# Kernel optimization log

Hardware: AMD Instinct MI355X
Metric: run time of the kernel (lower is better)

Reference implementation:

```python
import jax, jax.numpy as jnp
import numpy as np

D_MODEL = 1024
N_HEADS = 16
MAX_LAG = 512
D_K = D_MODEL // N_HEADS


def setup_inputs() -> dict:
    key = jax.random.key(0)
    ks = jax.random.split(key, 11)
    B, S = 2, 2048
    x = jax.random.normal(ks[0], (B, S, D_MODEL), dtype=jnp.float32)
    lag = jax.random.randint(ks[1], (S,), 0, MAX_LAG + 1, dtype=jnp.int64)
    scale = 1.0 / np.sqrt(D_MODEL)
    wq = jax.random.normal(ks[2], (D_MODEL, D_MODEL), dtype=jnp.float32) * scale
    bq = jnp.zeros((D_MODEL,), dtype=jnp.float32)
    wk = jax.random.normal(ks[3], (D_MODEL, D_MODEL), dtype=jnp.float32) * scale
    bk = jnp.zeros((D_MODEL,), dtype=jnp.float32)
    wv = jax.random.normal(ks[4], (D_MODEL, D_MODEL), dtype=jnp.float32) * scale
    bv = jnp.zeros((D_MODEL,), dtype=jnp.float32)
    wo = jax.random.normal(ks[5], (D_MODEL, D_MODEL), dtype=jnp.float32) * scale
    bo = jnp.zeros((D_MODEL,), dtype=jnp.float32)
    lag_bias = jax.random.normal(ks[6], (N_HEADS, MAX_LAG + 1), dtype=jnp.float32) * 0.02
    return {"x": x, "lag": lag, "wq": wq, "bq": bq, "wk": wk, "bk": bk,
            "wv": wv, "bv": bv, "wo": wo, "bo": bo, "lag_bias": lag_bias}


def reference(x, lag, wq, bq, wk, bk, wv, bv, wo, bo, lag_bias):
    B, S, D = x.shape
    H, dk = N_HEADS, D_K
    # projections: torch Linear is x @ W.T + b; here weights stored as (in, out)
    q = (x @ wq + bq).reshape(B, S, H, dk).transpose(0, 2, 1, 3)  # (B,H,S,dk)
    k = (x @ wk + bk).reshape(B, S, H, dk).transpose(0, 2, 1, 3)
    v = (x @ wv + bv).reshape(B, S, H, dk).transpose(0, 2, 1, 3)
    scores = jnp.einsum('bhqd,bhkd->bhqk', q, k) / jnp.sqrt(jnp.float32(dk))
    ld = jnp.abs(lag[:, None] - lag[None, :]).astype(jnp.int32)  # (S,S)
    bias = lag_bias[:, ld]  # (H,S,S)
    attn = jax.nn.softmax(scores + bias[None], axis=-1)
    out = jnp.einsum('bhqk,bhkd->bhqd', attn, v)
    out = out.transpose(0, 2, 1, 3).reshape(B, S, D)
    return out @ wo + bo
```

## Files before the change

kernel.cpp:

```cpp
#include <hip/hip_runtime.h>

typedef __bf16 bf16;
typedef __bf16 bf16x8 __attribute__((ext_vector_type(8)));
typedef float f32x4 __attribute__((ext_vector_type(4)));

__device__ __forceinline__ f32x4 mfma16(bf16x8 a, bf16x8 b, f32x4 c) {
  return __builtin_amdgcn_mfma_f32_16x16x32_bf16(a, b, c, 0, 0, 0);
}
__device__ __forceinline__ void gload16(const bf16* g, bf16* l) {
  __builtin_amdgcn_global_load_lds((const __attribute__((address_space(1))) unsigned int*)g,
                                   (__attribute__((address_space(3))) unsigned int*)l, 16, 0, 0);
}

__global__ __launch_bounds__(256) void cvt_x_kernel(const float* __restrict__ in,
                                                    bf16* __restrict__ out, int n8) {
  int i = blockIdx.x * 256 + threadIdx.x;
  if (i >= n8) return;
  const float4* p = (const float4*)in + (size_t)i * 2;
  float4 f0 = p[0], f1 = p[1];
  bf16x8 o;
  o[0] = (bf16)f0.x; o[1] = (bf16)f0.y; o[2] = (bf16)f0.z; o[3] = (bf16)f0.w;
  o[4] = (bf16)f1.x; o[5] = (bf16)f1.y; o[6] = (bf16)f1.z; o[7] = (bf16)f1.w;
  *((bf16x8*)out + i) = o;
}

__global__ __launch_bounds__(256) void cvt_wt_kernel(const float* __restrict__ in,
                                                     bf16* __restrict__ out) {
  __shared__ float t[64][68];
  int bx = blockIdx.x & 15;
  int by = blockIdx.x >> 4;
  int tid = threadIdx.x;
  int r = tid >> 2, p = tid & 3;
  const float* src = in + (size_t)(by * 64 + r) * 1024 + bx * 64 + p * 16;
#pragma unroll
  for (int j = 0; j < 16; j += 4)
    *(float4*)&t[r][p * 16 + j] = *(const float4*)(src + j);
  __syncthreads();
  int n = tid >> 2, sp = tid & 3;
  bf16 tmp[16];
#pragma unroll
  for (int j = 0; j < 16; ++j) tmp[j] = (bf16)t[sp * 16 + j][n];
  bf16* dst = out + (size_t)(bx * 64 + n) * 1024 + by * 64 + sp * 16;
  *(bf16x8*)dst = *(bf16x8*)&tmp[0];
  *(bf16x8*)(dst + 8) = *(bf16x8*)&tmp[8];
}

__global__ void cvt_bias_kernel(const float* __restrict__ bq, const float* __restrict__ bk,
                                const float* __restrict__ bv, float* __restrict__ out) {
  int i = blockIdx.x * 256 + threadIdx.x;
  if (i < 1024) out[i] = bq[i];
  else if (i < 2048) out[i] = bk[i - 1024];
  else if (i < 3072) out[i] = bv[i - 2048];
}

__global__ __launch_bounds__(256) void sort_lag_kernel(const int* __restrict__ lag,
                                                       int* __restrict__ perm,
                                                       int* __restrict__ slag) {
  __shared__ int l[2048];
  int tid = threadIdx.x;
  for (int i = tid; i < 2048; i += 256) l[i] = lag[i];
  __syncthreads();
  int i = blockIdx.x * 32 + (tid >> 3);
  int s = tid & 7;
  int vi = l[i];
  int cnt = 0;
  for (int j = s * 256; j < s * 256 + 256; j += 4) {
    int4 vj = *(const int4*)&l[j];
    cnt += (vj.x < vi || (vj.x == vi && (j + 0) < i));
    cnt += (vj.y < vi || (vj.y == vi && (j + 1) < i));
    cnt += (vj.z < vi || (vj.z == vi && (j + 2) < i));
    cnt += (vj.w < vi || (vj.w == vi && (j + 3) < i));
  }
  cnt += __shfl_xor(cnt, 1);
  cnt += __shfl_xor(cnt, 2);
  cnt += __shfl_xor(cnt, 4);
  if (s == 0) { perm[cnt] = i; slag[cnt] = vi; }
}

__global__ __launch_bounds__(256) void pack_kv_kernel(const bf16* __restrict__ qkv,
                                                      const int* __restrict__ perm,
                                                      bf16* __restrict__ kp,
                                                      bf16* __restrict__ vt) {
  __shared__ bf16 t[64][72];
  int blk = blockIdx.x;
  int st = blk & 31, h = (blk >> 5) & 15, b = blk >> 9;
  int tid = threadIdx.x;
  int r = tid >> 2, p = tid & 3;
  int src_s = perm[st * 64 + r];
  {
    const bf16* src = qkv + (size_t)(b * 2048 + src_s) * 3072 + 1024 + h * 64 + p * 16;
    bf16* dst = kp + (size_t)((b * 16 + h) * 2048 + st * 64 + r) * 64 + p * 16;
    *(bf16x8*)dst = *(const bf16x8*)src;
    *(bf16x8*)(dst + 8) = *(const bf16x8*)(src + 8);
  }
  {
    const bf16* src = qkv + (size_t)(b * 2048 + src_s) * 3072 + 2048 + h * 64 + p * 16;
    *(bf16x8*)&t[r][p * 16] = *(const bf16x8*)src;
    *(bf16x8*)&t[r][p * 16 + 8] = *(const bf16x8*)(src + 8);
    __syncthreads();
    int d = tid >> 2, sp = tid & 3;
    bf16 tmp[16];
#pragma unroll
    for (int j = 0; j < 16; ++j) tmp[j] = t[sp * 16 + j][d];
    bf16* dst = vt + (size_t)((b * 16 + h) * 64 + d) * 2048 + st * 64 + sp * 16;
    *(bf16x8*)dst = *(bf16x8*)&tmp[0];
    *(bf16x8*)(dst + 8) = *(bf16x8*)&tmp[8];
  }
}

template <int OUT_BF16>
__global__ __launch_bounds__(256) void gemm_bt_kernel(
    const bf16* __restrict__ A, const bf16* __restrict__ Bt,
    const float* __restrict__ bias, void* __restrict__ C,
    int M, int N, int K, int scale_cols, float scale_val) {
  __shared__ __align__(16) bf16 As[128 * 64];
  __shared__ __align__(16) bf16 Bs[128 * 64];
  int bn = blockIdx.x * 128, bm = blockIdx.y * 128;
  int tid = threadIdx.x;
  int l = tid & 63;
  int w = tid >> 6;
  int wr = w >> 1, wc = w & 1;
  int g = l >> 4, c = l & 15;
  int swz = (c & 7) << 3;
  int srow = l >> 3;
  int scol = ((l & 7) ^ srow) << 3;
  const bf16* Ap = A + (size_t)(bm + w * 32 + srow) * K + scol;
  const bf16* Bp = Bt + (size_t)(bn + w * 32 + srow) * K + scol;
  bf16* AsW = As + w * 32 * 64;
  bf16* BsW = Bs + w * 32 * 64;

  f32x4 acc[4][4] = {};
  for (int k0 = 0; k0 < K; k0 += 64) {
    __syncthreads();
#pragma unroll
    for (int i = 0; i < 4; ++i) {
      gload16(Ap + (size_t)(8 * i) * K + k0, AsW + i * 512);
      gload16(Bp + (size_t)(8 * i) * K + k0, BsW + i * 512);
    }
    __syncthreads();
#pragma unroll
    for (int kh = 0; kh < 2; ++kh) {
      bf16x8 af[4], bfr[4];
#pragma unroll
      for (int m = 0; m < 4; ++m)
        af[m] = *(const bf16x8*)&As[(wr * 64 + m * 16 + c) * 64 + ((kh * 32 + g * 8) ^ swz)];
#pragma unroll
      for (int n = 0; n < 4; ++n)
        bfr[n] = *(const bf16x8*)&Bs[(wc * 64 + n * 16 + c) * 64 + ((kh * 32 + g * 8) ^ swz)];
#pragma unroll
      for (int m = 0; m < 4; ++m)
#pragma unroll
        for (int n = 0; n < 4; ++n)
          acc[m][n] = mfma16(af[m], bfr[n], acc[m][n]);
    }
  }
  int rowb = bm + wr * 64;
  int colb = bn + wc * 64;
#pragma unroll
  for (int n = 0; n < 4; ++n) {
    int col = colb + n * 16 + c;
    float bv = bias[col];
    float s = (col < scale_cols) ? scale_val : 1.0f;
#pragma unroll
    for (int m = 0; m < 4; ++m) {
      int row = rowb + m * 16 + g * 4;
#pragma unroll
      for (int j = 0; j < 4; ++j) {
        float v = (acc[m][n][j] + bv) * s;
        if (OUT_BF16)
          ((bf16*)C)[(size_t)(row + j) * N + col] = (bf16)v;
        else
          ((float*)C)[(size_t)(row + j) * N + col] = v;
      }
    }
  }
}

__global__ __launch_bounds__(256) void attn_kernel(
    const bf16* __restrict__ qkv, const bf16* __restrict__ kp,
    const bf16* __restrict__ vt, const int* __restrict__ lag,
    const int* __restrict__ slag, const float* __restrict__ lag_bias,
    bf16* __restrict__ out) {
  __shared__ __align__(16) bf16 Ks0[64 * 64];
  __shared__ __align__(16) bf16 Vs0[64 * 64];
  __shared__ __align__(16) bf16 Ks1[64 * 64];
  __shared__ __align__(16) bf16 Vs1[64 * 64];
  __shared__ __align__(16) bf16 Ps[4][32][72];
  __shared__ float bias_s[516];
  __shared__ int lag_s[2048];

  int blk = blockIdx.x;
  blk = (blk & 7) * 64 + (blk >> 3);
  int qt = blk & 15;
  int h = (blk >> 4) & 15;
  int b = blk >> 8;
  int tid = threadIdx.x;
  int w = tid >> 6, l = tid & 63, g = l >> 4, c = l & 15;

  for (int i = tid; i < 513; i += 256) bias_s[i] = lag_bias[h * 513 + i] * 1.44269504f;
  for (int i = tid; i < 2048; i += 256) lag_s[i] = slag[i];

  int q0 = qt * 128 + w * 32;
  const bf16* qbase = qkv + (size_t)(b * 2048 + q0) * 3072 + h * 64;
  bf16x8 qf[2][2];
#pragma unroll
  for (int m = 0; m < 2; ++m)
#pragma unroll
    for (int kh = 0; kh < 2; ++kh)
      qf[m][kh] = *(const bf16x8*)(qbase + (size_t)(m * 16 + c) * 3072 + kh * 32 + g * 8);

  int lagq[2][4];
#pragma unroll
  for (int m = 0; m < 2; ++m)
#pragma unroll
    for (int j = 0; j < 4; ++j) lagq[m][j] = lag[q0 + m * 16 + g * 4 + j];

  int swz = (c & 7) << 3;
  int off0 = (g * 8) ^ swz;
  int off1 = off0 ^ 32;

  int r0 = w * 16 + (l >> 3);
  int colE = ((l & 7) ^ (l >> 3)) << 3;
  const bf16* kbase = kp + (size_t)(b * 16 + h) * 2048 * 64;
  const bf16* vbase = vt + (size_t)(b * 16 + h) * 64 * 2048;
  const bf16* kg0 = kbase + (size_t)r0 * 64 + colE;
  const bf16* kg1 = kbase + (size_t)(r0 + 8) * 64 + colE;
  const bf16* vg0 = vbase + (size_t)r0 * 2048 + colE;
  const bf16* vg1 = vbase + (size_t)(r0 + 8) * 2048 + colE;

#define STAGE(KD, VD)                    \
  do {                                   \
    gload16(kg0, KD + w * 1024);         \
    gload16(kg1, KD + w * 1024 + 512);   \
    gload16(vg0, VD + w * 1024);         \
    gload16(vg1, VD + w * 1024 + 512);   \
    kg0 += 64 * 64; kg1 += 64 * 64;      \
    vg0 += 64; vg1 += 64;                \
  } while (0)

  STAGE(Ks0, Vs0);
  __syncthreads();

  f32x4 oacc[2][4] = {};
  float psum[2][4] = {};

#define TILE(KB, VB, KT)                                                          \
  do {                                                                            \
    f32x4 sf[2][4] = {};                                                          \
    int lagk[4];                                                                  \
    _Pragma("unroll") for (int kb = 0; kb < 4; ++kb) {                            \
      int row = kb * 16 + c;                                                      \
      bf16x8 k0 = *(const bf16x8*)&KB[row * 64 + off0];                           \
      bf16x8 k1 = *(const bf16x8*)&KB[row * 64 + off1];                           \
      sf[0][kb] = mfma16(qf[0][0], k0, sf[0][kb]);                                \
      sf[0][kb] = mfma16(qf[0][1], k1, sf[0][kb]);                                \
      sf[1][kb] = mfma16(qf[1][0], k0, sf[1][kb]);                                \
      sf[1][kb] = mfma16(qf[1][1], k1, sf[1][kb]);                                \
      lagk[kb] = lag_s[(KT) + kb * 16 + c];                                       \
    }                                                                             \
    _Pragma("unroll") for (int m = 0; m < 2; ++m)                                 \
    _Pragma("unroll") for (int kb = 0; kb < 4; ++kb)                              \
    _Pragma("unroll") for (int j = 0; j < 4; ++j) {                               \
      int ld = lagq[m][j] - lagk[kb];                                             \
      ld = ld < 0 ? -ld : ld;                                                     \
      float p = __builtin_amdgcn_exp2f(sf[m][kb][j] + bias_s[ld]);                \
      psum[m][j] += p;                                                            \
      Ps[w][m * 16 + g * 4 + j][kb * 16 + c] = (bf16)p;                           \
    }                                                                             \
    asm volatile("s_waitcnt lgkmcnt(0)" ::: "memory");                            \
    _Pragma("unroll") for (int ph = 0; ph < 2; ++ph) {                            \
      bf16x8 pa0 = *(const bf16x8*)&Ps[w][c][ph * 32 + g * 8];                    \
      bf16x8 pa1 = *(const bf16x8*)&Ps[w][16 + c][ph * 32 + g * 8];               \
      int voff = ph ? off1 : off0;                                                \
      _Pragma("unroll") for (int n = 0; n < 4; ++n) {                             \
        bf16x8 vf = *(const bf16x8*)&VB[(n * 16 + c) * 64 + voff];                \
        oacc[0][n] = mfma16(pa0, vf, oacc[0][n]);                                 \
        oacc[1][n] = mfma16(pa1, vf, oacc[1][n]);                                 \
      }                                                                           \
    }                                                                             \
  } while (0)

  for (int kt = 0; kt < 2048; kt += 128) {
    if (kt + 64 < 2048) STAGE(Ks1, Vs1);
    TILE(Ks0, Vs0, kt);
    __syncthreads();
    if (kt + 128 < 2048) STAGE(Ks0, Vs0);
    TILE(Ks1, Vs1, kt + 64);
    __syncthreads();
  }

#pragma unroll
  for (int m = 0; m < 2; ++m) {
#pragma unroll
    for (int j = 0; j < 4; ++j) {
      float s = psum[m][j];
      s += __shfl_xor(s, 1);
      s += __shfl_xor(s, 2);
      s += __shfl_xor(s, 4);
      s += __shfl_xor(s, 8);
      float inv = 1.f / s;
      bf16* ob = out + (size_t)(b * 2048 + q0 + m * 16 + g * 4 + j) * 1024 + h * 64;
#pragma unroll
      for (int n = 0; n < 4; ++n)
        ob[n * 16 + c] = (bf16)(oacc[m][n][j] * inv);
    }
  }
#undef STAGE
#undef TILE
}

extern "C" void kernel_launch(void* const* d_in, const int* in_sizes, int n_in,
                              void* d_out, int out_size, void* d_ws, size_t ws_size,
                              hipStream_t stream) {
  const float* x        = (const float*)d_in[0];
  const int*   lag      = (const int*)d_in[1];
  const float* wq       = (const float*)d_in[2];
  const float* bq       = (const float*)d_in[3];
  const float* wk       = (const float*)d_in[4];
  const float* bk       = (const float*)d_in[5];
  const float* wv       = (const float*)d_in[6];
  const float* bv       = (const float*)d_in[7];
  const float* wo       = (const float*)d_in[8];
  const float* bo       = (const float*)d_in[9];
  const float* lag_bias = (const float*)d_in[10];

  char* ws = (char*)d_ws;
  bf16*  xb    = (bf16*)ws;
  bf16*  wqkvt = (bf16*)(ws + (8u  << 20));
  bf16*  wot   = (bf16*)(ws + (14u << 20));
  float* bqkv  = (float*)(ws + (16u << 20));
  int*   perm  = (int*)(ws + (16u << 20) + 32768);
  int*   slag  = (int*)(ws + (16u << 20) + 65536);
  bf16*  qkv   = (bf16*)(ws + (17u << 20));
  bf16*  vtb   = (bf16*)(ws + (41u << 20));
  bf16*  aout  = (bf16*)(ws + (49u << 20));
  bf16*  kpk   = xb;

  sort_lag_kernel<<<64, 256, 0, stream>>>(lag, perm, slag);
  cvt_x_kernel<<<2048, 256, 0, stream>>>(x, xb, 524288);
  cvt_wt_kernel<<<256, 256, 0, stream>>>(wq, wqkvt);
  cvt_wt_kernel<<<256, 256, 0, stream>>>(wk, wqkvt + (1u << 20));
  cvt_wt_kernel<<<256, 256, 0, stream>>>(wv, wqkvt + (2u << 20));
  cvt_wt_kernel<<<256, 256, 0, stream>>>(wo, wot);
  cvt_bias_kernel<<<12, 256, 0, stream>>>(bq, bk, bv, bqkv);
  gemm_bt_kernel<1><<<dim3(24, 32), 256, 0, stream>>>(
      xb, wqkvt, bqkv, qkv, 4096, 3072, 1024, 1024, 0.125f * 1.44269504f);
  pack_kv_kernel<<<1024, 256, 0, stream>>>(qkv, perm, kpk, vtb);
  attn_kernel<<<512, 256, 0, stream>>>(qkv, kpk, vtb, lag, slag, lag_bias, aout);
  gemm_bt_kernel<0><<<dim3(8, 32), 256, 0, stream>>>(
      aout, wot, bo, (float*)d_out, 4096, 1024, 1024, 0, 1.0f);
}
```

Before: 182.0 us.

## Fuse prep conversions into one launch, add smaller-tile output GEMM, drop abs in bias lookup

Merges the x conversion, the four weight transpose-conversions and the bias copy into a single prep kernel, cutting five launches and their gaps. Replaces the output projection GEMM with a dedicated 64x128-tile kernel so the grid doubles to 512 blocks and fills more CUs. In attention, it stores a mirrored bias table indexed by lag difference plus 512, which removes the abs operation from the inner softmax loop at the cost of a larger shared table. The new GEMM is single-buffered and syncs twice per k-step, so it may lose some overlap.

```diff
diff --git a/kernel.cpp b/kernel.cpp
--- a/kernel.cpp
+++ b/kernel.cpp
@@ -12,24 +12,40 @@
                                    (__attribute__((address_space(3))) unsigned int*)l, 16, 0, 0);
 }
 
-__global__ __launch_bounds__(256) void cvt_x_kernel(const float* __restrict__ in,
-                                                    bf16* __restrict__ out, int n8) {
-  int i = blockIdx.x * 256 + threadIdx.x;
-  if (i >= n8) return;
-  const float4* p = (const float4*)in + (size_t)i * 2;
-  float4 f0 = p[0], f1 = p[1];
-  bf16x8 o;
-  o[0] = (bf16)f0.x; o[1] = (bf16)f0.y; o[2] = (bf16)f0.z; o[3] = (bf16)f0.w;
-  o[4] = (bf16)f1.x; o[5] = (bf16)f1.y; o[6] = (bf16)f1.z; o[7] = (bf16)f1.w;
-  *((bf16x8*)out + i) = o;
-}
-
-__global__ __launch_bounds__(256) void cvt_wt_kernel(const float* __restrict__ in,
-                                                     bf16* __restrict__ out) {
+__global__ __launch_bounds__(256) void prep_kernel(
+    const float* __restrict__ x, const float* __restrict__ wq,
+    const float* __restrict__ wk, const float* __restrict__ wv,
+    const float* __restrict__ wo, const float* __restrict__ bq,
+    const float* __restrict__ bk, const float* __restrict__ bv,
+    bf16* __restrict__ xb, bf16* __restrict__ wqkvt, bf16* __restrict__ wot,
+    float* __restrict__ bqkv) {
+  int blk = blockIdx.x;
+  int tid = threadIdx.x;
+  if (blk < 2048) {
+    int i = blk * 256 + tid;
+    const float4* p = (const float4*)x + (size_t)i * 2;
+    float4 f0 = p[0], f1 = p[1];
+    bf16x8 o;
+    o[0] = (bf16)f0.x; o[1] = (bf16)f0.y; o[2] = (bf16)f0.z; o[3] = (bf16)f0.w;
+    o[4] = (bf16)f1.x; o[5] = (bf16)f1.y; o[6] = (bf16)f1.z; o[7] = (bf16)f1.w;
+    *((bf16x8*)xb + i) = o;
+    return;
+  }
+  if (blk >= 3072) {
+    int i = (blk - 3072) * 256 + tid;
+    if (i < 1024) bqkv[i] = bq[i];
+    else if (i < 2048) bqkv[i] = bk[i - 1024];
+    else if (i < 3072) bqkv[i] = bv[i - 2048];
+    return;
+  }
   __shared__ float t[64][68];
-  int bx = blockIdx.x & 15;
-  int by = blockIdx.x >> 4;
-  int tid = threadIdx.x;
+  int sub = blk - 2048;
+  int wsel = sub >> 8;
+  sub &= 255;
+  const float* in = wsel == 0 ? wq : wsel == 1 ? wk : wsel == 2 ? wv : wo;
+  bf16* out = (wsel == 3) ? wot : (wqkvt + (size_t)wsel * (1u << 20));
+  int bx = sub & 15;
+  int by = sub >> 4;
   int r = tid >> 2, p = tid & 3;
   const float* src = in + (size_t)(by * 64 + r) * 1024 + bx * 64 + p * 16;
 #pragma unroll
@@ -43,14 +59,6 @@
   bf16* dst = out + (size_t)(bx * 64 + n) * 1024 + by * 64 + sp * 16;
   *(bf16x8*)dst = *(bf16x8*)&tmp[0];
   *(bf16x8*)(dst + 8) = *(bf16x8*)&tmp[8];
-}
-
-__global__ void cvt_bias_kernel(const float* __restrict__ bq, const float* __restrict__ bk,
-                                const float* __restrict__ bv, float* __restrict__ out) {
-  int i = blockIdx.x * 256 + threadIdx.x;
-  if (i < 1024) out[i] = bq[i];
-  else if (i < 2048) out[i] = bk[i - 1024];
-  else if (i < 3072) out[i] = bv[i - 2048];
 }
 
 __global__ __launch_bounds__(256) void sort_lag_kernel(const int* __restrict__ lag,
@@ -176,6 +184,66 @@
   }
 }
 
+__global__ __launch_bounds__(256) void gemm64_kernel(
+    const bf16* __restrict__ A, const bf16* __restrict__ Bt,
+    const float* __restrict__ bias, float* __restrict__ C,
+    int M, int N, int K) {
+  __shared__ __align__(16) bf16 As[64 * 64];
+  __shared__ __align__(16) bf16 Bs[128 * 64];
+  int bn = blockIdx.x * 128, bm = blockIdx.y * 64;
+  int tid = threadIdx.x;
+  int l = tid & 63;
+  int w = tid >> 6;
+  int g = l >> 4, c = l & 15;
+  int swz = (c & 7) << 3;
+  int srow = l >> 3;
+  int scol = ((l & 7) ^ srow) << 3;
+  const bf16* Ap = A + (size_t)(bm + w * 16 + srow) * K + scol;
+  const bf16* Bp = Bt + (size_t)(bn + w * 32 + srow) * K + scol;
+  bf16* AsW = As + w * 16 * 64;
+  bf16* BsW = Bs + w * 32 * 64;
+
+  f32x4 acc[4][2] = {};
+  for (int k0 = 0; k0 < K; k0 += 64) {
+    __syncthreads();
+#pragma unroll
+    for (int i = 0; i < 2; ++i)
+      gload16(Ap + (size_t)(8 * i) * K + k0, AsW + i * 512);
+#pragma unroll
+    for (int i = 0; i < 4; ++i)
+      gload16(Bp + (size_t)(8 * i) * K + k0, BsW + i * 512);
+    __syncthreads();
+#pragma unroll
+    for (int kh = 0; kh < 2; ++kh) {
+      int koff = (kh * 32 + g * 8) ^ swz;
+      bf16x8 af[4], bfr[2];
+#pragma unroll
+      for (int m = 0; m < 4; ++m)
+        af[m] = *(const bf16x8*)&As[(m * 16 + c) * 64 + koff];
+#pragma unroll
+      for (int n = 0; n < 2; ++n)
+        bfr[n] = *(const bf16x8*)&Bs[(w * 32 + n * 16 + c) * 64 + koff];
+#pragma unroll
+      for (int m = 0; m < 4; ++m)
+#pragma unroll
+        for (int n = 0; n < 2; ++n)
+          acc[m][n] = mfma16(af[m], bfr[n], acc[m][n]);
+    }
+  }
+#pragma unroll
+  for (int n = 0; n < 2; ++n) {
+    int col = bn + w * 32 + n * 16 + c;
+    float bv = bias[col];
+#pragma unroll
+    for (int m = 0; m < 4; ++m) {
+      int row = bm + m * 16 + g * 4;
+#pragma unroll
+      for (int j = 0; j < 4; ++j)
+        C[(size_t)(row + j) * N + col] = acc[m][n][j] + bv;
+    }
+  }
+}
+
 __global__ __launch_bounds__(256) void attn_kernel(
     const bf16* __restrict__ qkv, const bf16* __restrict__ kp,
     const bf16* __restrict__ vt, const int* __restrict__ lag,
@@ -186,7 +254,7 @@
   __shared__ __align__(16) bf16 Ks1[64 * 64];
   __shared__ __align__(16) bf16 Vs1[64 * 64];
   __shared__ __align__(16) bf16 Ps[4][32][72];
-  __shared__ float bias_s[516];
+  __shared__ float bias2_s[1028];
   __shared__ int lag_s[2048];
 
   int blk = blockIdx.x;
@@ -197,7 +265,11 @@
   int tid = threadIdx.x;
   int w = tid >> 6, l = tid & 63, g = l >> 4, c = l & 15;
 
-  for (int i = tid; i < 513; i += 256) bias_s[i] = lag_bias[h * 513 + i] * 1.44269504f;
+  for (int i = tid; i < 1025; i += 256) {
+    int d = i - 512;
+    d = d < 0 ? -d : d;
+    bias2_s[i] = lag_bias[h * 513 + d] * 1.44269504f;
+  }
   for (int i = tid; i < 2048; i += 256) lag_s[i] = slag[i];
 
   int q0 = qt * 128 + w * 32;
@@ -213,7 +285,7 @@
 #pragma unroll
   for (int m = 0; m < 2; ++m)
 #pragma unroll
-    for (int j = 0; j < 4; ++j) lagq[m][j] = lag[q0 + m * 16 + g * 4 + j];
+    for (int j = 0; j < 4; ++j) lagq[m][j] = lag[q0 + m * 16 + g * 4 + j] + 512;
 
   int swz = (c & 7) << 3;
   int off0 = (g * 8) ^ swz;
@@ -262,8 +334,7 @@
     _Pragma("unroll") for (int kb = 0; kb < 4; ++kb)                              \
     _Pragma("unroll") for (int j = 0; j < 4; ++j) {                               \
       int ld = lagq[m][j] - lagk[kb];                                             \
-      ld = ld < 0 ? -ld : ld;                                                     \
-      float p = __builtin_amdgcn_exp2f(sf[m][kb][j] + bias_s[ld]);                \
+      float p = __builtin_amdgcn_exp2f(sf[m][kb][j] + bias2_s[ld]);               \
       psum[m][j] += p;                                                            \
       Ps[w][m * 16 + g * 4 + j][kb * 16 + c] = (bf16)p;                           \
     }                                                                             \
@@ -337,16 +408,12 @@
   bf16*  kpk   = xb;
 
   sort_lag_kernel<<<64, 256, 0, stream>>>(lag, perm, slag);
-  cvt_x_kernel<<<2048, 256, 0, stream>>>(x, xb, 524288);
-  cvt_wt_kernel<<<256, 256, 0, stream>>>(wq, wqkvt);
-  cvt_wt_kernel<<<256, 256, 0, stream>>>(wk, wqkvt + (1u << 20));
-  cvt_wt_kernel<<<256, 256, 0, stream>>>(wv, wqkvt + (2u << 20));
-  cvt_wt_kernel<<<256, 256, 0, stream>>>(wo, wot);
-  cvt_bias_kernel<<<12, 256, 0, stream>>>(bq, bk, bv, bqkv);
+  prep_kernel<<<3084, 256, 0, stream>>>(x, wq, wk, wv, wo, bq, bk, bv,
+                                        xb, wqkvt, wot, bqkv);
   gemm_bt_kernel<1><<<dim3(24, 32), 256, 0, stream>>>(
       xb, wqkvt, bqkv, qkv, 4096, 3072, 1024, 1024, 0.125f * 1.44269504f);
   pack_kv_kernel<<<1024, 256, 0, stream>>>(qkv, perm, kpk, vtb);
   attn_kernel<<<512, 256, 0, stream>>>(qkv, kpk, vtb, lag, slag, lag_bias, aout);
-  gemm_bt_kernel<0><<<dim3(8, 32), 256, 0, stream>>>(
-      aout, wot, bo, (float*)d_out, 4096, 1024, 1024, 0, 1.0f);
-}
+  gemm64_kernel<<<dim3(8, 64), 256, 0, stream>>>(
+      aout, wot, bo, (float*)d_out, 4096, 1024, 1024);
+}
```

After: 161.7 us. 11.1% less time.
